# Optimization experiments

Measured on AMD Instinct MI355X. Metric: run time of the kernel, lower is better.

The kernel has to match this reference:

```python
import jax, jax.numpy as jnp
import numpy as np

NUM_HEADS = 16
NEG_INF = -1e30


def setup_inputs() -> dict:
    key = jax.random.key(0)
    k1, k2, k3 = jax.random.split(key, 3)
    B, S, D = 2, 2048, 1024
    x = jax.random.normal(k1, (B, S, D), dtype=jnp.float32)
    # torch Linear(D, 3D, bias=False) stored here already transposed: y = x @ w_qkv
    w_qkv = jax.random.normal(k2, (D, 3 * D), dtype=jnp.float32) * 0.02
    w_out = jax.random.normal(k3, (D, D), dtype=jnp.float32) * 0.02
    return {"x": x, "w_qkv": w_qkv, "w_out": w_out}


def reference(x, w_qkv, w_out):
    B, S, D = x.shape
    H = NUM_HEADS
    dh = D // H
    qkv = x @ w_qkv                      # [B, S, 3D]
    q, k, v = jnp.split(qkv, 3, axis=-1)

    def to_heads(t):
        return t.reshape(B, S, H, dh).transpose(0, 2, 1, 3)  # [B, H, S, dh]

    q, k, v = to_heads(q), to_heads(k), to_heads(v)
    scale = jnp.asarray(dh, x.dtype) ** -0.5
    scores = jnp.einsum('bhqd,bhkd->bhqk', q, k) * scale     # [B, H, S, S]
    causal = jnp.tril(jnp.ones((S, S), dtype=bool))
    scores = jnp.where(causal, scores, NEG_INF)
    attn = jax.nn.softmax(scores, axis=-1)
    out = jnp.einsum('bhqk,bhkd->bhqd', attn, v)             # [B, H, S, dh]
    out = out.transpose(0, 2, 1, 3).reshape(B, S, D)
    return out @ w_out
```

## Files before the change

kernel.cpp:

```cpp
#include <hip/hip_runtime.h>

typedef unsigned short u16;
typedef unsigned int u32;

typedef __bf16 bf16x8 __attribute__((ext_vector_type(8)));
typedef _Float16 f16x8 __attribute__((ext_vector_type(8)));
typedef float f32x4 __attribute__((ext_vector_type(4)));
typedef float f32x16 __attribute__((ext_vector_type(16)));
typedef u32 u32x4 __attribute__((ext_vector_type(4)));

typedef __attribute__((address_space(1))) u32 as1_u32;
typedef __attribute__((address_space(3))) u32 as3_u32;

#define EKF 0.18033688011112042f

__device__ __forceinline__ u16 f2bf(float x) {
  u32 u = __float_as_uint(x);
  u = u + 0x7fffu + ((u >> 16) & 1u);
  return (u16)(u >> 16);
}
__device__ __forceinline__ u32 pack2(float a, float b) {
  return (u32)f2bf(a) | ((u32)f2bf(b) << 16);
}
__device__ __forceinline__ u32 pkf16(float a, float b) {
  return __builtin_bit_cast(u32, __builtin_amdgcn_cvt_pkrtz(a, b));
}
__device__ __forceinline__ u16 f2h(float a) {
  return (u16)(pkf16(a, a) & 0xffffu);
}
__device__ __forceinline__ void gld_lds16(const u16* g, const u16* l) {
  __builtin_amdgcn_global_load_lds((const as1_u32*)g, (as3_u32*)l, 16, 0, 0);
}

__global__ __launch_bounds__(256) void prepass_kernel(const float* __restrict__ x,
                                                      const float* __restrict__ w_qkv,
                                                      const float* __restrict__ w_out,
                                                      u16* __restrict__ xb,
                                                      u16* __restrict__ wqkvT,
                                                      u16* __restrict__ woutT) {
  __shared__ float tile[64][65];
  int bid = blockIdx.x;
  int t = threadIdx.x;
  if (bid < 4096) {
    int i = bid * 256 + t;
    float4 v = ((const float4*)x)[i];
    uint2 r;
    r.x = pack2(v.x, v.y);
    r.y = pack2(v.z, v.w);
    ((uint2*)xb)[i] = r;
    return;
  }
  const float* W;
  u16* WT;
  int K, N, bx, by;
  if (bid < 4096 + 768) {
    int b2 = bid - 4096;
    W = w_qkv; WT = wqkvT; K = 1024; N = 3072; bx = b2 & 15; by = b2 >> 4;
  } else {
    int b2 = bid - 4864;
    W = w_out; WT = woutT; K = 1024; N = 1024; bx = b2 & 15; by = b2 >> 4;
  }
  int k0 = bx * 64, n0 = by * 64;
  int r = t >> 4, c4 = (t & 15) * 4;
#pragma unroll
  for (int i = 0; i < 4; ++i) {
    int row = r + i * 16;
    float4 v = *(const float4*)&W[(size_t)(k0 + row) * N + n0 + c4];
    tile[row][c4 + 0] = v.x; tile[row][c4 + 1] = v.y;
    tile[row][c4 + 2] = v.z; tile[row][c4 + 3] = v.w;
  }
  __syncthreads();
#pragma unroll
  for (int i = 0; i < 4; ++i) {
    int n = r + i * 16;
    uint2 o;
    o.x = pack2(tile[c4 + 0][n], tile[c4 + 1][n]);
    o.y = pack2(tile[c4 + 2][n], tile[c4 + 3][n]);
    *(uint2*)&WT[(size_t)(n0 + n) * K + k0 + c4] = o;
  }
}

__global__ __launch_bounds__(512, 2) void gemm_qkv256_kernel(const u16* __restrict__ A,
                                                             const u16* __restrict__ BT,
                                                             u16* __restrict__ QK,
                                                             u16* __restrict__ VT) {
  __shared__ __attribute__((aligned(16))) u16 smem[65536];
  const int tid = threadIdx.x;
  const int wave = tid >> 6;
  const int lane = tid & 63;
  const int lr = lane & 15;
  const int kg = lane >> 4;
  const int l7 = lr & 7;
  const int wr = wave >> 2;
  const int wc = wave & 3;

  int b = blockIdx.x;
  int sw = (b & 7) * 24 + (b >> 3);
  const int bn = (sw % 12) * 256;
  const int bm = (sw / 12) * 256;

  const int srow = tid >> 3;
  const int scg = ((tid & 7) ^ (srow & 7)) * 8;
  const u16* pa = A + (size_t)(bm + srow) * 1024 + scg;
  const u16* pb = BT + (size_t)(bn + srow) * 1024 + scg;
  const u32 lw = (u32)wave * 512;

  f32x4 acc[8][4];
#pragma unroll
  for (int i = 0; i < 8; ++i)
#pragma unroll
    for (int j = 0; j < 4; ++j) {
      f32x4 z = {0.f, 0.f, 0.f, 0.f};
      acc[i][j] = z;
    }

  {
    u16* dA = (u16*)smem;
    u16* dB = (u16*)smem + 16384;
#pragma unroll
    for (int i = 0; i < 4; ++i) gld_lds16(pa + (size_t)(i * 64) * 1024, dA + lw + i * 4096);
#pragma unroll
    for (int i = 0; i < 4; ++i) gld_lds16(pb + (size_t)(i * 64) * 1024, dB + lw + i * 4096);
  }

  for (int t = 0; t < 16; ++t) {
    __syncthreads();
    const u16* bA = smem + (t & 1) * 32768;
    const u16* bB = bA + 16384;
    if (t + 1 < 16) {
      u16* dA = (u16*)smem + ((t + 1) & 1) * 32768;
      u16* dB = dA + 16384;
      const int k1 = (t + 1) * 64;
#pragma unroll
      for (int i = 0; i < 4; ++i) gld_lds16(pa + (size_t)(i * 64) * 1024 + k1, dA + lw + i * 4096);
#pragma unroll
      for (int i = 0; i < 4; ++i) gld_lds16(pb + (size_t)(i * 64) * 1024 + k1, dB + lw + i * 4096);
    }
    bf16x8 bfr[2][4];
#pragma unroll
    for (int kh = 0; kh < 2; ++kh)
#pragma unroll
      for (int ni = 0; ni < 4; ++ni)
        bfr[kh][ni] = *(const bf16x8*)(bB + (wc * 64 + ni * 16 + lr) * 64 +
                                       (((kh * 4 + kg) ^ l7) * 8));
#pragma unroll
    for (int ph = 0; ph < 4; ++ph) {
      const int mh = ph >> 1, kh = ph & 1;
      bf16x8 af[4];
#pragma unroll
      for (int mi = 0; mi < 4; ++mi)
        af[mi] = *(const bf16x8*)(bA + (wr * 128 + mh * 64 + mi * 16 + lr) * 64 +
                                  (((kh * 4 + kg) ^ l7) * 8));
      __builtin_amdgcn_s_barrier();
      __builtin_amdgcn_s_setprio(1);
#pragma unroll
      for (int mi = 0; mi < 4; ++mi)
#pragma unroll
        for (int ni = 0; ni < 4; ++ni)
          acc[mh * 4 + mi][ni] = __builtin_amdgcn_mfma_f32_16x16x32_bf16(
              bfr[kh][ni], af[mi], acc[mh * 4 + mi][ni], 0, 0, 0);
      __builtin_amdgcn_s_setprio(0);
      __builtin_amdgcn_s_barrier();
    }
  }

  __syncthreads();
  if (bn >= 2048) {
#pragma unroll
    for (int mi = 0; mi < 8; ++mi)
#pragma unroll
      for (int ni = 0; ni < 4; ++ni) {
        int r = bm + wr * 128 + mi * 16 + lr;
        int c = bn + wc * 64 + ni * 16 + kg * 4 - 2048;
        int bh2 = (r >> 11) * 16 + (c >> 6);
        int j = r & 2047;
        u16* vrow = VT + ((size_t)bh2 * 64 + (c & 63)) * 2048 + j;
        f32x4 a = acc[mi][ni];
#pragma unroll
        for (int rr = 0; rr < 4; ++rr) vrow[(size_t)rr * 2048] = f2h(a[rr]);
      }
  } else {
    float scale = (bn < 1024) ? EKF : 1.0f;
#pragma unroll
    for (int mi = 0; mi < 8; ++mi)
#pragma unroll
      for (int ni = 0; ni < 4; ++ni) {
        int row = wr * 128 + mi * 16 + lr;
        u32 off = (u32)row * 256 + wc * 64 + (((ni * 4 + kg) ^ (lr & 6)) * 4);
        f32x4 a = acc[mi][ni];
        *(uint2*)((u16*)smem + off) =
            make_uint2(pack2(a[0] * scale, a[1] * scale), pack2(a[2] * scale, a[3] * scale));
      }
    __syncthreads();
#pragma unroll
    for (int i = 0; i < 16; ++i) {
      int row = i * 16 + (tid >> 5);
      int lc = tid & 31;
      int blk = lc >> 3, cc = lc & 7;
      uint4 v = *(const uint4*)((const u16*)smem + (u32)row * 256 + blk * 64 +
                                (((2 * cc) ^ (row & 6)) * 4));
      *(uint4*)(QK + (size_t)(bm + row) * 2048 + bn + blk * 64 + cc * 8) = v;
    }
  }
}

__global__ __launch_bounds__(256, 2) void gemm_out_kernel(const u16* __restrict__ A,
                                                          const u16* __restrict__ BT,
                                                          float* __restrict__ C) {
  __shared__ __attribute__((aligned(16))) u16 smem[2][12288];
  const int tid = threadIdx.x;
  const int wave = tid >> 6;
  const int lane = tid & 63;
  const int lr = lane & 15;
  const int kg = lane >> 4;
  const int lr7 = lr & 7;
  const int wm = (wave >> 1) * 32;
  const int wn = (wave & 1) * 64;

  const int b = blockIdx.x;
  const int xcd = b & 7, loc = b >> 3;
  const int bm = (xcd * 8 + (loc >> 3)) * 64;
  const int bn = (loc & 7) * 128;

  const int sr = tid >> 3;
  const int scg = ((tid & 7) ^ (sr & 7)) * 8;
  const u16* pa = A + (size_t)(bm + sr) * 1024 + scg;
  const u16* pb = BT + (size_t)(bn + sr) * 1024 + scg;
  const u32 lw = (u32)wave * 512;

  f32x4 acc[2][4];
#pragma unroll
  for (int i = 0; i < 2; ++i)
#pragma unroll
    for (int j = 0; j < 4; ++j) {
      f32x4 z = {0.f, 0.f, 0.f, 0.f};
      acc[i][j] = z;
    }

  {
    u16* dA = smem[0];
    u16* dB = smem[0] + 4096;
#pragma unroll
    for (int i = 0; i < 2; ++i) gld_lds16(pa + (size_t)(i * 32) * 1024, dA + lw + i * 2048);
#pragma unroll
    for (int i = 0; i < 4; ++i) gld_lds16(pb + (size_t)(i * 32) * 1024, dB + lw + i * 2048);
  }

  for (int t = 0; t < 16; ++t) {
    __syncthreads();
    const u16* bA = smem[t & 1];
    const u16* bB = bA + 4096;
    if (t + 1 < 16) {
      u16* dA = smem[(t + 1) & 1];
      u16* dB = dA + 4096;
      const int k1 = (t + 1) * 64;
#pragma unroll
      for (int i = 0; i < 2; ++i) gld_lds16(pa + (size_t)(i * 32) * 1024 + k1, dA + lw + i * 2048);
#pragma unroll
      for (int i = 0; i < 4; ++i) gld_lds16(pb + (size_t)(i * 32) * 1024 + k1, dB + lw + i * 2048);
    }
#pragma unroll
    for (int kk = 0; kk < 2; ++kk) {
      const int ch = ((kk * 4 + kg) ^ lr7) * 8;
      bf16x8 af[2], bfr[4];
#pragma unroll
      for (int mi = 0; mi < 2; ++mi)
        af[mi] = *(const bf16x8*)(bA + (wm + mi * 16 + lr) * 64 + ch);
#pragma unroll
      for (int ni = 0; ni < 4; ++ni)
        bfr[ni] = *(const bf16x8*)(bB + (wn + ni * 16 + lr) * 64 + ch);
      __builtin_amdgcn_s_setprio(1);
#pragma unroll
      for (int mi = 0; mi < 2; ++mi)
#pragma unroll
        for (int ni = 0; ni < 4; ++ni)
          acc[mi][ni] = __builtin_amdgcn_mfma_f32_16x16x32_bf16(bfr[ni], af[mi], acc[mi][ni], 0, 0, 0);
      __builtin_amdgcn_s_setprio(0);
    }
  }

  float* buf = (float*)smem;
#pragma unroll
  for (int hc = 0; hc < 2; ++hc) {
    __syncthreads();
    if ((wave & 1) == hc) {
#pragma unroll
      for (int mi = 0; mi < 2; ++mi)
#pragma unroll
        for (int ni = 0; ni < 4; ++ni) {
          int row = wm + mi * 16 + lr;
          int cp = ((ni * 4 + kg) ^ lr) * 4;
          *(f32x4*)(buf + row * 64 + cp) = acc[mi][ni];
        }
    }
    __syncthreads();
#pragma unroll
    for (int i = 0; i < 4; ++i) {
      int row = i * 16 + (tid >> 4);
      int lc = tid & 15;
      float4 v = *(const float4*)(buf + row * 64 + ((lc ^ (row & 15)) * 4));
      *(float4*)(C + (size_t)(bm + row) * 1024 + bn + hc * 64 + lc * 4) = v;
    }
  }
}

__global__ __launch_bounds__(256, 4) void attn_mfma_kernel(const u16* __restrict__ qk,
                                                           const u16* __restrict__ vt,
                                                           u16* __restrict__ out) {
  __shared__ __attribute__((aligned(16))) u16 sK[2][64 * 64];
  __shared__ __attribute__((aligned(16))) u16 sV[2][64 * 64];

  const int tid = threadIdx.x;
  const int wave = tid >> 6;
  const int lane = tid & 63;
  const int l31 = lane & 31;
  const int hi = lane >> 5;
  const int qh = wave & 1;
  const int jh = wave >> 1;

  int idx = blockIdx.x;
  int qi = 31 - (idx >> 5);
  int bh = (idx & 7) * 4 + ((idx >> 3) & 3);
  int b = bh >> 4, h = bh & 15;
  int q0 = qi * 64;

  const u16* qbase = qk + (size_t)b * 2048 * 2048 + h * 64;
  const u16* kbase = qbase + 1024;
  const u16* vbase = vt + (size_t)bh * 64 * 2048;
  u16* obase = out + (size_t)b * 2048 * 1024 + h * 64;

  const int sra = wave * 16 + (lane >> 3);
  const int srb = sra + 8;
  const int sc = lane & 7;
  const u32 koffA = (u32)sra * 2048 + (u32)((sc ^ (sra & 7)) * 8);
  const u32 koffB = (u32)srb * 2048 + (u32)((sc ^ (srb & 7)) * 8);
  const u32 ldsA = (wave * 2 + 0) * 512;
  const u32 ldsB = (wave * 2 + 1) * 512;

  const int qcol = q0 + qh * 32 + l31;
  bf16x8 qf[4];
  {
    const u16* qrow = qbase + (size_t)qcol * 2048;
#pragma unroll
    for (int s = 0; s < 4; ++s) qf[s] = *(const bf16x8*)(qrow + s * 16 + hi * 8);
  }

  f32x16 oacc[2];
#pragma unroll
  for (int i = 0; i < 16; ++i) { oacc[0][i] = 0.f; oacc[1][i] = 0.f; }
  float ls = 0.f;

  const int nrounds = qi + 1;
  gld_lds16(kbase + koffA, sK[0] + ldsA);
  gld_lds16(kbase + koffB, sK[0] + ldsB);
  gld_lds16(vbase + koffA, sV[0] + ldsA);
  gld_lds16(vbase + koffB, sV[0] + ldsB);
  __syncthreads();

  for (int t = 0; t < nrounds; ++t) {
    if (t + 1 < nrounds) {
      int j1 = (t + 1) * 64;
      u16* dK = sK[(t + 1) & 1];
      u16* dV = sV[(t + 1) & 1];
      gld_lds16(kbase + (size_t)j1 * 2048 + koffA, dK + ldsA);
      gld_lds16(kbase + (size_t)j1 * 2048 + koffB, dK + ldsB);
      gld_lds16(vbase + j1 + koffA, dV + ldsA);
      gld_lds16(vbase + j1 + koffB, dV + ldsB);
    }
    const u16* sKb = sK[t & 1];
    const u16* sVb = sV[t & 1];
    const bool diag = (t == qi);

    f32x16 c;
#pragma unroll
    for (int i = 0; i < 16; ++i) c[i] = 0.f;
#pragma unroll
    for (int s = 0; s < 4; ++s) {
      const u32 row = (u32)(jh * 32 + l31);
      bf16x8 kf = *(const bf16x8*)(sKb + row * 64 + (((2 * s + hi) ^ (row & 7)) * 8));
      c = __builtin_amdgcn_mfma_f32_32x32x16_bf16(kf, qf[s], c, 0, 0, 0);
    }
    float p[16];
    const int qrel = qh * 32 + l31;
#pragma unroll
    for (int r = 0; r < 16; ++r) {
      int joff = jh * 32 + (r & 3) + 8 * (r >> 2) + 4 * hi;
      float e = exp2f(c[r]);
      p[r] = (!diag || (joff <= qrel)) ? e : 0.f;
    }
    {
      float s0 = (p[0] + p[1]) + (p[2] + p[3]);
      float s1 = (p[4] + p[5]) + (p[6] + p[7]);
      float s2 = (p[8] + p[9]) + (p[10] + p[11]);
      float s3 = (p[12] + p[13]) + (p[14] + p[15]);
      ls += (s0 + s1) + (s2 + s3);
    }
    u32 c01 = pkf16(p[0], p[1]),   c23 = pkf16(p[2], p[3]);
    u32 c45 = pkf16(p[4], p[5]),   c67 = pkf16(p[6], p[7]);
    u32 c89 = pkf16(p[8], p[9]),   cab = pkf16(p[10], p[11]);
    u32 ccd = pkf16(p[12], p[13]), cef = pkf16(p[14], p[15]);
    asm volatile("v_permlane32_swap_b32 %0, %1" : "+v"(c01), "+v"(c45));
    asm volatile("v_permlane32_swap_b32 %0, %1" : "+v"(c23), "+v"(c67));
    asm volatile("v_permlane32_swap_b32 %0, %1" : "+v"(c89), "+v"(ccd));
    asm volatile("v_permlane32_swap_b32 %0, %1" : "+v"(cab), "+v"(cef));
    u32x4 w0 = {c01, c23, c45, c67};
    u32x4 w1 = {c89, cab, ccd, cef};
    f16x8 pa0 = __builtin_bit_cast(f16x8, w0);
    f16x8 pa1 = __builtin_bit_cast(f16x8, w1);

    __builtin_amdgcn_s_setprio(1);
#pragma unroll
    for (int dh = 0; dh < 2; ++dh) {
      const u32 row = (u32)(dh * 32 + l31);
#pragma unroll
      for (int s2 = 0; s2 < 2; ++s2) {
        f16x8 vf = *(const f16x8*)(sVb + row * 64 +
                                   (((4 * jh + 2 * s2 + hi) ^ (row & 7)) * 8));
        oacc[dh] = __builtin_amdgcn_mfma_f32_32x32x16_f16(
            vf, (s2 == 0) ? pa0 : pa1, oacc[dh], 0, 0, 0);
      }
    }
    __builtin_amdgcn_s_setprio(0);
    __syncthreads();
  }

  ls += __shfl_xor(ls, 32);

  float* obuf = (float*)sK;
  float* lbuf = (float*)sV;
  const int q = qh * 32 + l31;
  if (jh == 1) {
#pragma unroll
    for (int dh = 0; dh < 2; ++dh)
#pragma unroll
      for (int g = 0; g < 4; ++g) {
        int ch = dh * 8 + g * 2 + hi;
        f32x4 w = {oacc[dh][4 * g + 0], oacc[dh][4 * g + 1],
                   oacc[dh][4 * g + 2], oacc[dh][4 * g + 3]};
        *(f32x4*)(obuf + q * 64 + ((ch ^ (q & 15)) * 4)) = w;
      }
    if (hi == 0) lbuf[q] = ls;
  }
  __syncthreads();
  if (jh == 0) {
    float inv = 1.0f / (ls + lbuf[q]);
    u16* orow = obase + (size_t)qcol * 1024;
#pragma unroll
    for (int dh = 0; dh < 2; ++dh)
#pragma unroll
      for (int g = 0; g < 4; ++g) {
        int ch = dh * 8 + g * 2 + hi;
        f32x4 po = *(const f32x4*)(obuf + q * 64 + ((ch ^ (q & 15)) * 4));
        float o0 = (oacc[dh][4 * g + 0] + po[0]) * inv;
        float o1 = (oacc[dh][4 * g + 1] + po[1]) * inv;
        float o2 = (oacc[dh][4 * g + 2] + po[2]) * inv;
        float o3 = (oacc[dh][4 * g + 3] + po[3]) * inv;
        *(uint2*)(orow + dh * 32 + g * 8 + hi * 4) = make_uint2(pack2(o0, o1), pack2(o2, o3));
      }
  }
}

extern "C" void kernel_launch(void* const* d_in, const int* in_sizes, int n_in,
                              void* d_out, int out_size, void* d_ws, size_t ws_size,
                              hipStream_t stream) {
  const float* x = (const float*)d_in[0];
  const float* w_qkv = (const float*)d_in[1];
  const float* w_out = (const float*)d_in[2];
  float* out = (float*)d_out;

  char* ws = (char*)d_ws;
  u16* xb    = (u16*)(ws);
  u16* wqkvT = (u16*)(ws + (8u << 20));
  u16* woutT = (u16*)(ws + (14u << 20));
  u16* qkb   = (u16*)(ws + (16u << 20));
  u16* vtb   = (u16*)(ws + (32u << 20));
  u16* attn  = (u16*)(ws + (40u << 20));

  prepass_kernel<<<5120, 256, 0, stream>>>(x, w_qkv, w_out, xb, wqkvT, woutT);

  gemm_qkv256_kernel<<<192, 512, 0, stream>>>(xb, wqkvT, qkb, vtb);

  attn_mfma_kernel<<<1024, 256, 0, stream>>>(qkb, vtb, attn);

  gemm_out_kernel<<<512, 256, 0, stream>>>(attn, woutT, out);
}
```

Before: 162.5 us.

## Retile QKV GEMM to 256x192 tiles to fill all CUs

Changes the QKV projection GEMM from 256x256 tiles (192 blocks) to 256x192 tiles (256 blocks), so the grid matches the CU count of the MI355X. Each wave now covers 48 columns instead of 64, and the shared-memory footprint shrinks. Because tiles can now straddle the Q/K/V boundaries, the epilogue decides per fragment whether to write transposed V or scaled Q/K through LDS. The cost is lower arithmetic intensity per block and per-element branching in the epilogue.

```diff
diff --git a/kernel.cpp b/kernel.cpp
--- a/kernel.cpp
+++ b/kernel.cpp
@@ -84,7 +84,7 @@
                                                              const u16* __restrict__ BT,
                                                              u16* __restrict__ QK,
                                                              u16* __restrict__ VT) {
-  __shared__ __attribute__((aligned(16))) u16 smem[65536];
+  __shared__ __attribute__((aligned(16))) u16 smem[57344];
   const int tid = threadIdx.x;
   const int wave = tid >> 6;
   const int lane = tid & 63;
@@ -95,9 +95,9 @@
   const int wc = wave & 3;
 
   int b = blockIdx.x;
-  int sw = (b & 7) * 24 + (b >> 3);
-  const int bn = (sw % 12) * 256;
-  const int bm = (sw / 12) * 256;
+  int sw = (b & 7) * 32 + (b >> 3);
+  const int bm = (sw >> 4) * 256;
+  const int bn = (sw & 15) * 192;
 
   const int srow = tid >> 3;
   const int scg = ((tid & 7) ^ (srow & 7)) * 8;
@@ -105,11 +105,11 @@
   const u16* pb = BT + (size_t)(bn + srow) * 1024 + scg;
   const u32 lw = (u32)wave * 512;
 
-  f32x4 acc[8][4];
+  f32x4 acc[8][3];
 #pragma unroll
   for (int i = 0; i < 8; ++i)
 #pragma unroll
-    for (int j = 0; j < 4; ++j) {
+    for (int j = 0; j < 3; ++j) {
       f32x4 z = {0.f, 0.f, 0.f, 0.f};
       acc[i][j] = z;
     }
@@ -120,28 +120,28 @@
 #pragma unroll
     for (int i = 0; i < 4; ++i) gld_lds16(pa + (size_t)(i * 64) * 1024, dA + lw + i * 4096);
 #pragma unroll
-    for (int i = 0; i < 4; ++i) gld_lds16(pb + (size_t)(i * 64) * 1024, dB + lw + i * 4096);
+    for (int i = 0; i < 3; ++i) gld_lds16(pb + (size_t)(i * 64) * 1024, dB + lw + i * 4096);
   }
 
   for (int t = 0; t < 16; ++t) {
     __syncthreads();
-    const u16* bA = smem + (t & 1) * 32768;
+    const u16* bA = smem + (t & 1) * 28672;
     const u16* bB = bA + 16384;
     if (t + 1 < 16) {
-      u16* dA = (u16*)smem + ((t + 1) & 1) * 32768;
+      u16* dA = (u16*)smem + ((t + 1) & 1) * 28672;
       u16* dB = dA + 16384;
       const int k1 = (t + 1) * 64;
 #pragma unroll
       for (int i = 0; i < 4; ++i) gld_lds16(pa + (size_t)(i * 64) * 1024 + k1, dA + lw + i * 4096);
 #pragma unroll
-      for (int i = 0; i < 4; ++i) gld_lds16(pb + (size_t)(i * 64) * 1024 + k1, dB + lw + i * 4096);
-    }
-    bf16x8 bfr[2][4];
+      for (int i = 0; i < 3; ++i) gld_lds16(pb + (size_t)(i * 64) * 1024 + k1, dB + lw + i * 4096);
+    }
+    bf16x8 bfr[2][3];
 #pragma unroll
     for (int kh = 0; kh < 2; ++kh)
 #pragma unroll
-      for (int ni = 0; ni < 4; ++ni)
-        bfr[kh][ni] = *(const bf16x8*)(bB + (wc * 64 + ni * 16 + lr) * 64 +
+      for (int ni = 0; ni < 3; ++ni)
+        bfr[kh][ni] = *(const bf16x8*)(bB + (wc * 48 + ni * 16 + lr) * 64 +
                                        (((kh * 4 + kg) ^ l7) * 8));
 #pragma unroll
     for (int ph = 0; ph < 4; ++ph) {
@@ -156,7 +156,7 @@
 #pragma unroll
       for (int mi = 0; mi < 4; ++mi)
 #pragma unroll
-        for (int ni = 0; ni < 4; ++ni)
+        for (int ni = 0; ni < 3; ++ni)
           acc[mh * 4 + mi][ni] = __builtin_amdgcn_mfma_f32_16x16x32_bf16(
               bfr[kh][ni], af[mi], acc[mh * 4 + mi][ni], 0, 0, 0);
       __builtin_amdgcn_s_setprio(0);
@@ -165,41 +165,41 @@
   }
 
   __syncthreads();
-  if (bn >= 2048) {
-#pragma unroll
-    for (int mi = 0; mi < 8; ++mi)
-#pragma unroll
-      for (int ni = 0; ni < 4; ++ni) {
-        int r = bm + wr * 128 + mi * 16 + lr;
-        int c = bn + wc * 64 + ni * 16 + kg * 4 - 2048;
-        int bh2 = (r >> 11) * 16 + (c >> 6);
+#pragma unroll
+  for (int i = 0; i < 8; ++i)
+#pragma unroll
+    for (int ni = 0; ni < 3; ++ni) {
+      const int coff = wc * 48 + ni * 16 + kg * 4;
+      const int cglob = bn + coff;
+      f32x4 a = acc[i][ni];
+      if (cglob >= 2048) {
+        int r = bm + wr * 128 + i * 16 + lr;
+        int cc = cglob - 2048;
+        int bh2 = (r >> 11) * 16 + (cc >> 6);
         int j = r & 2047;
-        u16* vrow = VT + ((size_t)bh2 * 64 + (c & 63)) * 2048 + j;
-        f32x4 a = acc[mi][ni];
+        u16* vrow = VT + ((size_t)bh2 * 64 + (cc & 63)) * 2048 + j;
 #pragma unroll
         for (int rr = 0; rr < 4; ++rr) vrow[(size_t)rr * 2048] = f2h(a[rr]);
-      }
-  } else {
-    float scale = (bn < 1024) ? EKF : 1.0f;
-#pragma unroll
-    for (int mi = 0; mi < 8; ++mi)
-#pragma unroll
-      for (int ni = 0; ni < 4; ++ni) {
-        int row = wr * 128 + mi * 16 + lr;
-        u32 off = (u32)row * 256 + wc * 64 + (((ni * 4 + kg) ^ (lr & 6)) * 4);
-        f32x4 a = acc[mi][ni];
+      } else {
+        float scale = (cglob < 1024) ? EKF : 1.0f;
+        int row = wr * 128 + i * 16 + lr;
+        int chunk = coff >> 2;
+        u32 off = (u32)row * 192 + (u32)((chunk ^ (row & 6)) << 2);
         *(uint2*)((u16*)smem + off) =
             make_uint2(pack2(a[0] * scale, a[1] * scale), pack2(a[2] * scale, a[3] * scale));
       }
-    __syncthreads();
-#pragma unroll
-    for (int i = 0; i < 16; ++i) {
-      int row = i * 16 + (tid >> 5);
+    }
+  __syncthreads();
+  if (bn < 2048) {
+#pragma unroll
+    for (int i2 = 0; i2 < 16; ++i2) {
+      int row = i2 * 16 + (tid >> 5);
       int lc = tid & 31;
-      int blk = lc >> 3, cc = lc & 7;
-      uint4 v = *(const uint4*)((const u16*)smem + (u32)row * 256 + blk * 64 +
-                                (((2 * cc) ^ (row & 6)) * 4));
-      *(uint4*)(QK + (size_t)(bm + row) * 2048 + bn + blk * 64 + cc * 8) = v;
+      if (lc < 24 && bn + lc * 8 < 2048) {
+        uint4 v = *(const uint4*)((const u16*)smem + (u32)row * 192 +
+                                  (u32)(((2 * lc) ^ (row & 6)) * 4));
+        *(uint4*)(QK + (size_t)(bm + row) * 2048 + bn + lc * 8) = v;
+      }
     }
   }
 }
@@ -478,7 +478,7 @@
 
   prepass_kernel<<<5120, 256, 0, stream>>>(x, w_qkv, w_out, xb, wqkvT, woutT);
 
-  gemm_qkv256_kernel<<<192, 512, 0, stream>>>(xb, wqkvT, qkb, vtb);
+  gemm_qkv256_kernel<<<256, 512, 0, stream>>>(xb, wqkvT, qkb, vtb);
 
   attn_mfma_kernel<<<1024, 256, 0, stream>>>(qkb, vtb, attn);
 
```

New measurement: 160.5 us. No clear change (-1.2%).
